# Optimization experiments

Hardware: AMD Instinct MI355X
Metric: run time of the kernel (lower is better)

The kernel has to match this reference:

```python
import jax, jax.numpy as jnp
import numpy as np

B, P, D, C = 1024, 4, 512, 128  # batch, parts, feat_dim, num_classes


def setup_inputs() -> dict:
    key = jax.random.key(0)
    k1, k2 = jax.random.split(key)
    # scale 0.05 keeps dot products O(1) so exp() stays in fp32 range
    inputs = jax.random.normal(k1, (B, P, D), dtype=jnp.float32) * 0.05
    targets = jax.random.randint(k2, (B,), 0, C, dtype=jnp.int64)
    return {"inputs": inputs, "targets": targets}


def _npairs_loss(inputs, targets):
    b, p, d = inputs.shape
    n = b * p
    X = inputs.reshape(n, d)
    t = jnp.repeat(targets, p)              # (n,) class label per row
    parts = jnp.tile(jnp.arange(p), b)      # (n,) part id per row
    prod = X @ X.T                          # (n, n) similarities

    sc = t[:, None] == t[None, :]           # same class
    sp = parts[:, None] == parts[None, :]   # same attention part
    s_sadc = (~sc) & sp
    s_dasc = sc & (~sp)
    s_dadc = (~sc) & (~sp)

    e_pos = jnp.exp(prod)                   # exp(neg) terms
    e_neg = jnp.exp(-prod)                  # exp(-pos) terms

    def group_loss(pos_mask, neg_mask):
        # sum_i sum_{j in pos_i} log(1 + sum_{k in neg_i} exp(prod[i,k] - prod[i,j]))
        # = sum log1p(S_i * exp(-prod[i,j])) with S_i = sum_{k in neg_i} exp(prod[i,k])
        S = jnp.sum(jnp.where(neg_mask, e_pos, 0.0), axis=1)        # (n,)
        terms = jnp.where(pos_mask, jnp.log1p(S[:, None] * e_neg), 0.0)
        return jnp.sum(terms)

    loss_sadc = group_loss(s_sadc, s_dadc)
    loss_dasc = group_loss(s_dasc, s_dadc)
    # NOTE: original returns loss_sadc twice and never uses loss_sasc (bug kept for fidelity)
    return (loss_sadc + loss_sadc + loss_dasc) / n


def reference(inputs, targets):
    return _npairs_loss(inputs, targets)
```

## Files before the change

### kernel.cpp

```cpp
#include <hip/hip_runtime.h>
#include <stdint.h>

#define GLOBAL_AS __attribute__((address_space(1)))
#define LDS_AS    __attribute__((address_space(3)))

typedef __attribute__((ext_vector_type(8))) __bf16 bf16x8;
typedef __attribute__((ext_vector_type(4))) float  f32x4;

static_assert(sizeof(bf16x8) == 16, "bf16x8 must be 16B");

constexpr int N  = 4096;
constexpr int DK = 512;


__global__ void k_convert(const float* __restrict__ X, __bf16* __restrict__ Xb) {
    int idx = blockIdx.x * blockDim.x + threadIdx.x;
    const float4* s = (const float4*)X;
    float4 a = s[2 * idx + 0];
    float4 b = s[2 * idx + 1];
    bf16x8 o;
    o[0] = (__bf16)a.x; o[1] = (__bf16)a.y; o[2] = (__bf16)a.z; o[3] = (__bf16)a.w;
    o[4] = (__bf16)b.x; o[5] = (__bf16)b.y; o[6] = (__bf16)b.z; o[7] = (__bf16)b.w;
    *(bf16x8*)(Xb + 8 * idx) = o;
}

__global__ void k_cls(const int* __restrict__ tbuf, int* __restrict__ cls) {
    __shared__ int is64;
    int t = threadIdx.x;
    if (t == 0) is64 = 1;
    __syncthreads();
    if (t < 512 && tbuf[2 * t + 1] != 0) is64 = 0;
    __syncthreads();
    int idx = is64 ? (2 * t) : t;
    int v = tbuf[idx];
    cls[4 * t + 0] = v;
    cls[4 * t + 1] = v;
    cls[4 * t + 2] = v;
    cls[4 * t + 3] = v;
}

__launch_bounds__(256, 3)
__global__ void k_main(const __bf16* __restrict__ Xb, const int* __restrict__ cls,
                       float* __restrict__ partials) {
    __shared__ __align__(16) __bf16 As[128 * 64];
    __shared__ __align__(16) __bf16 Bs[128 * 64];
    __shared__ float accS[128], accP[128], accE[128], accW[128];
    __shared__ int rowcls[128], colcls[128];

    const int tid  = threadIdx.x;
    const int lane = tid & 63;
    const int wid  = tid >> 6;
    const int rt = blockIdx.x & 31;
    const int g  = blockIdx.x >> 5;
    const int i0 = rt * 128;
    const int j0 = g * 128;

    if (tid < 128) {
        rowcls[tid] = cls[i0 + tid];
        colcls[tid] = cls[j0 + tid];
        accS[tid] = 0.f; accP[tid] = 0.f; accE[tid] = 0.f; accW[tid] = 0.f;
    }

    const int wr = wid >> 1;
    const int wc = wid & 1;

    f32x4 acc[4][4] = {};

    const char* xb   = (const char*)Xb;
    const int   srow = tid >> 3;
    const int   skb  = (tid & 7) * 16;
    char* AsB = (char*)As;
    char* BsB = (char*)Bs;
    const int ldsOff = wid * 1024;

    const int rA   = lane & 15;
    const int kgrp = lane >> 4;

    for (int kt = 0; kt < DK / 64; ++kt) {
        const size_t kb0 = (size_t)kt * 128;
#pragma unroll
        for (int t = 0; t < 4; ++t) {
            __builtin_amdgcn_global_load_lds(
                (const GLOBAL_AS void*)(xb + (size_t)(i0 + t * 32 + srow) * 1024 + kb0 + skb),
                (LDS_AS void*)(AsB + t * 4096 + ldsOff), 16, 0, 0);
            __builtin_amdgcn_global_load_lds(
                (const GLOBAL_AS void*)(xb + (size_t)(j0 + t * 32 + srow) * 1024 + kb0 + skb),
                (LDS_AS void*)(BsB + t * 4096 + ldsOff), 16, 0, 0);
        }
        __syncthreads();
#pragma unroll
        for (int kk = 0; kk < 2; ++kk) {
            const int koff = kk * 64 + kgrp * 16;
            bf16x8 af[4], bg[4];
#pragma unroll
            for (int m = 0; m < 4; ++m)
                af[m] = *(const bf16x8*)(AsB + (wr * 64 + m * 16 + rA) * 128 + koff);
#pragma unroll
            for (int n = 0; n < 4; ++n)
                bg[n] = *(const bf16x8*)(BsB + (wc * 64 + n * 16 + rA) * 128 + koff);
#pragma unroll
            for (int m = 0; m < 4; ++m)
#pragma unroll
                for (int n = 0; n < 4; ++n)
                    acc[m][n] = __builtin_amdgcn_mfma_f32_16x16x32_bf16(af[m], bg[n],
                                                                        acc[m][n], 0, 0, 0);
        }
        __syncthreads();
    }

    const int pj = lane & 3;
#pragma unroll
    for (int m = 0; m < 4; ++m) {
        const int rbase = wr * 64 + m * 16 + kgrp * 4;
        int ci[4];
#pragma unroll
        for (int r = 0; r < 4; ++r) ci[r] = rowcls[rbase + r];
        float sS[4] = {0.f, 0.f, 0.f, 0.f};
        float sP[4] = {0.f, 0.f, 0.f, 0.f};
        float sE[4] = {0.f, 0.f, 0.f, 0.f};
        float sW[4] = {0.f, 0.f, 0.f, 0.f};
#pragma unroll
        for (int n = 0; n < 4; ++n) {
            const int cj = colcls[wc * 64 + n * 16 + rA];
#pragma unroll
            for (int r = 0; r < 4; ++r) {
                const float p  = acc[m][n][r];
                const float ep = __expf(p);
                const bool sc = (ci[r] == cj);
                const bool sp = (r == pj);
                if (!sc && !sp) sS[r] += ep;
                const float w = (!sc && sp) ? 2.f : ((sc && !sp) ? 1.f : 0.f);
                sP[r] += w * p;
                sE[r] += w * ep;
                sW[r] += w;
            }
        }
#pragma unroll
        for (int r = 0; r < 4; ++r) {
            float vS = sS[r], vP = sP[r], vE = sE[r], vW = sW[r];
#pragma unroll
            for (int off = 1; off < 16; off <<= 1) {
                vS += __shfl_xor(vS, off);
                vP += __shfl_xor(vP, off);
                vE += __shfl_xor(vE, off);
                vW += __shfl_xor(vW, off);
            }
            if (rA == 0) {
                const int row = rbase + r;
                atomicAdd(&accS[row], vS);
                atomicAdd(&accP[row], vP);
                atomicAdd(&accE[row], vE);
                atomicAdd(&accW[row], vW);
            }
        }
    }
    __syncthreads();
    if (tid < 128) {
        float4 o = make_float4(accS[tid], accP[tid], accE[tid], accW[tid]);
        ((float4*)partials)[(size_t)(i0 + tid) * 32 + g] = o;
    }
}

__global__ void k_rowloss(const float* __restrict__ partials, float* __restrict__ blockSums) {
    __shared__ float red[16];
    const int tid = threadIdx.x;
    const int sub = tid & 15;
    const int row = blockIdx.x * 16 + (tid >> 4);

    const float4* p = ((const float4*)partials) + (size_t)row * 32;
    float4 a = p[sub];
    float4 b = p[sub + 16];
    float S = a.x + b.x, P = a.y + b.y, E = a.z + b.z, W = a.w + b.w;
#pragma unroll
    for (int off = 1; off < 16; off <<= 1) {
        S += __shfl_xor(S, off);
        P += __shfl_xor(P, off);
        E += __shfl_xor(E, off);
        W += __shfl_xor(W, off);
    }
    if (sub == 0) red[tid >> 4] = W * logf(S) - P + E / S;
    __syncthreads();
    if (tid == 0) {
        float s = 0.f;
#pragma unroll
        for (int r = 0; r < 16; ++r) s += red[r];
        blockSums[blockIdx.x] = s;
    }
}

__global__ void k_final2(const float* __restrict__ blockSums, float* __restrict__ out) {
    const int t = threadIdx.x;
    float v = blockSums[t] + blockSums[t + 64] + blockSums[t + 128] + blockSums[t + 192];
#pragma unroll
    for (int off = 1; off < 64; off <<= 1) v += __shfl_xor(v, off);
    if (t == 0) out[0] = v / (float)N;
}

extern "C" void kernel_launch(void* const* d_in, const int* in_sizes, int n_in,
                              void* d_out, int out_size, void* d_ws, size_t ws_size,
                              hipStream_t stream) {
    const float* X = (const float*)d_in[0];
    const int*   T = (const int*)d_in[1];
    float* out = (float*)d_out;

    char* ws = (char*)d_ws;
    __bf16* Xb     = (__bf16*)ws;
    int*    cls    = (int*)(ws + (size_t)4 * 1024 * 1024);
    float*  parts  = (float*)(ws + (size_t)4 * 1024 * 1024 + 16 * 1024);
    float*  bsums  = (float*)ws;

    hipLaunchKernelGGL(k_convert, dim3((N * DK / 8) / 256), dim3(256), 0, stream, X, Xb);
    hipLaunchKernelGGL(k_cls,     dim3(1),    dim3(1024), 0, stream, T, cls);
    hipLaunchKernelGGL(k_main,    dim3(1024), dim3(256),  0, stream, Xb, cls, parts);
    hipLaunchKernelGGL(k_rowloss, dim3(256),  dim3(256),  0, stream, parts, bsums);
    hipLaunchKernelGGL(k_final2,  dim3(1),    dim3(64),   0, stream, bsums, out);
}
```

Measured before the change: 56.65 us.

## Exploit Gram symmetry with triangular tiles and double-buffer LDS staging

```diff
diff --git a/kernel.cpp b/kernel.cpp
--- a/kernel.cpp
+++ b/kernel.cpp
@@ -39,26 +39,33 @@
     cls[4 * t + 3] = v;
 }
 
-__launch_bounds__(256, 3)
+__launch_bounds__(256, 2)
 __global__ void k_main(const __bf16* __restrict__ Xb, const int* __restrict__ cls,
                        float* __restrict__ partials) {
-    __shared__ __align__(16) __bf16 As[128 * 64];
-    __shared__ __align__(16) __bf16 Bs[128 * 64];
+    __shared__ __align__(16) __bf16 As[2][128 * 64];
+    __shared__ __align__(16) __bf16 Bs[2][128 * 64];
     __shared__ float accS[128], accP[128], accE[128], accW[128];
+    __shared__ float accSc[128], accPc[128], accEc[128], accWc[128];
     __shared__ int rowcls[128], colcls[128];
 
     const int tid  = threadIdx.x;
     const int lane = tid & 63;
     const int wid  = tid >> 6;
-    const int rt = blockIdx.x & 31;
-    const int g  = blockIdx.x >> 5;
+
+    const int bid = blockIdx.x;
+    int rt = (int)((sqrtf(8.0f * (float)bid + 1.0f) - 1.0f) * 0.5f);
+    while (((rt + 1) * (rt + 2)) / 2 <= bid) ++rt;
+    while ((rt * (rt + 1)) / 2 > bid) --rt;
+    const int g  = bid - (rt * (rt + 1)) / 2;
     const int i0 = rt * 128;
     const int j0 = g * 128;
+    const bool offdiag = (rt != g);
 
     if (tid < 128) {
         rowcls[tid] = cls[i0 + tid];
         colcls[tid] = cls[j0 + tid];
-        accS[tid] = 0.f; accP[tid] = 0.f; accE[tid] = 0.f; accW[tid] = 0.f;
+        accS[tid] = 0.f;  accP[tid] = 0.f;  accE[tid] = 0.f;  accW[tid] = 0.f;
+        accSc[tid] = 0.f; accPc[tid] = 0.f; accEc[tid] = 0.f; accWc[tid] = 0.f;
     }
 
     const int wr = wid >> 1;
@@ -69,25 +76,36 @@
     const char* xb   = (const char*)Xb;
     const int   srow = tid >> 3;
     const int   skb  = (tid & 7) * 16;
-    char* AsB = (char*)As;
-    char* BsB = (char*)Bs;
     const int ldsOff = wid * 1024;
 
     const int rA   = lane & 15;
     const int kgrp = lane >> 4;
 
+#define STAGE(buf, kt)                                                                     \
+    {                                                                                      \
+        const size_t kb0 = (size_t)(kt) * 128;                                             \
+        char* AsB = (char*)(&As[(buf)][0]);                                                \
+        char* BsB = (char*)(&Bs[(buf)][0]);                                                \
+        _Pragma("unroll")                                                                  \
+        for (int t = 0; t < 4; ++t) {                                                      \
+            __builtin_amdgcn_global_load_lds(                                              \
+                (const GLOBAL_AS void*)(xb + (size_t)(i0 + t * 32 + srow) * 1024 + kb0 + skb), \
+                (LDS_AS void*)(AsB + t * 4096 + ldsOff), 16, 0, 0);                        \
+            __builtin_amdgcn_global_load_lds(                                              \
+                (const GLOBAL_AS void*)(xb + (size_t)(j0 + t * 32 + srow) * 1024 + kb0 + skb), \
+                (LDS_AS void*)(BsB + t * 4096 + ldsOff), 16, 0, 0);                        \
+        }                                                                                  \
+    }
+
+    STAGE(0, 0);
+    __syncthreads();
+
+    int cur = 0;
+#pragma unroll
     for (int kt = 0; kt < DK / 64; ++kt) {
-        const size_t kb0 = (size_t)kt * 128;
-#pragma unroll
-        for (int t = 0; t < 4; ++t) {
-            __builtin_amdgcn_global_load_lds(
-                (const GLOBAL_AS void*)(xb + (size_t)(i0 + t * 32 + srow) * 1024 + kb0 + skb),
-                (LDS_AS void*)(AsB + t * 4096 + ldsOff), 16, 0, 0);
-            __builtin_amdgcn_global_load_lds(
-                (const GLOBAL_AS void*)(xb + (size_t)(j0 + t * 32 + srow) * 1024 + kb0 + skb),
-                (LDS_AS void*)(BsB + t * 4096 + ldsOff), 16, 0, 0);
-        }
-        __syncthreads();
+        if (kt < DK / 64 - 1) STAGE(cur ^ 1, kt + 1);
+        const char* AsB = (const char*)(&As[cur][0]);
+        const char* BsB = (const char*)(&Bs[cur][0]);
 #pragma unroll
         for (int kk = 0; kk < 2; ++kk) {
             const int koff = kk * 64 + kgrp * 16;
@@ -105,10 +123,22 @@
                     acc[m][n] = __builtin_amdgcn_mfma_f32_16x16x32_bf16(af[m], bg[n],
                                                                         acc[m][n], 0, 0, 0);
         }
-        __syncthreads();
-    }
+        if (kt < DK / 64 - 1) {
+            __syncthreads();
+            cur ^= 1;
+        }
+    }
+#undef STAGE
 
     const int pj = lane & 3;
+    int cjv[4];
+#pragma unroll
+    for (int n = 0; n < 4; ++n) cjv[n] = colcls[wc * 64 + n * 16 + rA];
+    float cS[4] = {0.f, 0.f, 0.f, 0.f};
+    float cP[4] = {0.f, 0.f, 0.f, 0.f};
+    float cE[4] = {0.f, 0.f, 0.f, 0.f};
+    float cW[4] = {0.f, 0.f, 0.f, 0.f};
+
 #pragma unroll
     for (int m = 0; m < 4; ++m) {
         const int rbase = wr * 64 + m * 16 + kgrp * 4;
@@ -121,18 +151,18 @@
         float sW[4] = {0.f, 0.f, 0.f, 0.f};
 #pragma unroll
         for (int n = 0; n < 4; ++n) {
-            const int cj = colcls[wc * 64 + n * 16 + rA];
+            const int cj = cjv[n];
 #pragma unroll
             for (int r = 0; r < 4; ++r) {
                 const float p  = acc[m][n][r];
                 const float ep = __expf(p);
                 const bool sc = (ci[r] == cj);
                 const bool sp = (r == pj);
-                if (!sc && !sp) sS[r] += ep;
+                const bool dadc = (!sc && !sp);
+                if (dadc) { sS[r] += ep; cS[n] += ep; }
                 const float w = (!sc && sp) ? 2.f : ((sc && !sp) ? 1.f : 0.f);
-                sP[r] += w * p;
-                sE[r] += w * ep;
-                sW[r] += w;
+                sP[r] += w * p;  sE[r] += w * ep;  sW[r] += w;
+                cP[n] += w * p;  cE[n] += w * ep;  cW[n] += w;
             }
         }
 #pragma unroll
@@ -154,10 +184,33 @@
             }
         }
     }
+
+    if (offdiag) {
+#pragma unroll
+        for (int n = 0; n < 4; ++n) {
+            float vS = cS[n], vP = cP[n], vE = cE[n], vW = cW[n];
+            vS += __shfl_xor(vS, 16); vS += __shfl_xor(vS, 32);
+            vP += __shfl_xor(vP, 16); vP += __shfl_xor(vP, 32);
+            vE += __shfl_xor(vE, 16); vE += __shfl_xor(vE, 32);
+            vW += __shfl_xor(vW, 16); vW += __shfl_xor(vW, 32);
+            if (kgrp == 0) {
+                const int col = wc * 64 + n * 16 + rA;
+                atomicAdd(&accSc[col], vS);
+                atomicAdd(&accPc[col], vP);
+                atomicAdd(&accEc[col], vE);
+                atomicAdd(&accWc[col], vW);
+            }
+        }
+    }
+
     __syncthreads();
     if (tid < 128) {
         float4 o = make_float4(accS[tid], accP[tid], accE[tid], accW[tid]);
         ((float4*)partials)[(size_t)(i0 + tid) * 32 + g] = o;
+        if (offdiag) {
+            float4 oc = make_float4(accSc[tid], accPc[tid], accEc[tid], accWc[tid]);
+            ((float4*)partials)[(size_t)(j0 + tid) * 32 + rt] = oc;
+        }
     }
 }
 
@@ -210,8 +263,8 @@
     float*  bsums  = (float*)ws;
 
     hipLaunchKernelGGL(k_convert, dim3((N * DK / 8) / 256), dim3(256), 0, stream, X, Xb);
-    hipLaunchKernelGGL(k_cls,     dim3(1),    dim3(1024), 0, stream, T, cls);
-    hipLaunchKernelGGL(k_main,    dim3(1024), dim3(256),  0, stream, Xb, cls, parts);
-    hipLaunchKernelGGL(k_rowloss, dim3(256),  dim3(256),  0, stream, parts, bsums);
-    hipLaunchKernelGGL(k_final2,  dim3(1),    dim3(64),   0, stream, bsums, out);
-}
+    hipLaunchKernelGGL(k_cls,     dim3(1),   dim3(1024), 0, stream, T, cls);
+    hipLaunchKernelGGL(k_main,    dim3(528), dim3(256),  0, stream, Xb, cls, parts);
+    hipLaunchKernelGGL(k_rowloss, dim3(256), dim3(256),  0, stream, parts, bsums);
+    hipLaunchKernelGGL(k_final2,  dim3(1),   dim3(64),   0, stream, bsums, out);
+}
```

Result: no change. 56.65 us (-0.0%).
